# Optimization experiments

Hardware: AMD Instinct MI355X
Metric: run time of the kernel (lower is better)

Reference implementation:

```python
import jax, jax.numpy as jnp
import numpy as np

B, S, D, H = 2, 2048, 1024, 16
DK = D // H


def setup_inputs() -> dict:
    key = jax.random.key(0)
    ks = jax.random.split(key, 8)
    scale = 1.0 / np.sqrt(D)
    inp = {
        "query": jax.random.normal(ks[0], (B, S, D), dtype=jnp.float32),
        "key": jax.random.normal(ks[1], (B, S, D), dtype=jnp.float32),
        "value": jax.random.normal(ks[2], (B, S, D), dtype=jnp.float32),
        # causal mask, broadcastable over batch and heads
        "mask": jnp.tril(jnp.ones((S, S), dtype=jnp.int32))[None, None, :, :],
        "W_q": jax.random.normal(ks[3], (D, D), dtype=jnp.float32) * scale,
        "W_k": jax.random.normal(ks[4], (D, D), dtype=jnp.float32) * scale,
        "W_v": jax.random.normal(ks[5], (D, D), dtype=jnp.float32) * scale,
        "W_o": jax.random.normal(ks[6], (D, D), dtype=jnp.float32) * scale,
    }
    return inp


def _split_heads(t):
    Bb, Ss, _ = t.shape
    return t.reshape(Bb, Ss, H, DK).transpose(0, 2, 1, 3)  # [B,H,S,DK]


def reference(query, key, value, mask, W_q, W_k, W_v, W_o):
    # Linear(d,d,bias=False): y = x @ W^T (torch stores weight as [out,in])
    Q = _split_heads(query @ W_q.T)
    K = _split_heads(key @ W_k.T)
    V = _split_heads(value @ W_v.T)
    scores = jnp.einsum("bhqd,bhkd->bhqk", Q, K) / jnp.sqrt(jnp.float32(DK))
    scores = jnp.where(mask == 0, -jnp.inf, scores)
    weights = jax.nn.softmax(scores, axis=-1)
    weights = jnp.nan_to_num(weights, nan=0.0)  # fully-masked rows -> 0
    # dropout is identity at inference
    x = jnp.einsum("bhqk,bhkd->bhqd", weights, V)
    x = x.transpose(0, 2, 1, 3).reshape(B, S, D)
    return x @ W_o.T
```

## Files before the change

### kernel.cpp

```cpp
#include <hip/hip_runtime.h>
#include <hip/hip_bf16.h>

#define D_MODEL 1024
#define NHEAD   16
#define HDK     64
#define SEQ     2048
#define BATCH   2
#define BS      (BATCH * SEQ)

typedef __attribute__((ext_vector_type(8))) short bf16x8;
typedef __attribute__((ext_vector_type(4))) float f32x4;

__device__ __forceinline__ unsigned short f2bf(float f) {
    unsigned u = __builtin_bit_cast(unsigned, f);
    u += 0x7fffu + ((u >> 16) & 1u);
    return (unsigned short)(u >> 16);
}

__device__ __forceinline__ unsigned pack_hi(float x, float y) {
    return __builtin_amdgcn_perm(__builtin_bit_cast(unsigned, y),
                                 __builtin_bit_cast(unsigned, x), 0x07060302u);
}

typedef const void __attribute__((address_space(1))) gas_void;
typedef void __attribute__((address_space(3))) las_void;

__device__ __forceinline__ void gll16(const void* g, void* l) {
    __builtin_amdgcn_global_load_lds((gas_void*)g, (las_void*)l, 16, 0, 0);
}

__device__ __forceinline__ void cast_body(const float* __restrict__ src,
                                          unsigned short* __restrict__ dst, int i) {
    const float4* p = (const float4*)src + (size_t)i * 2;
    float4 a = p[0], b = p[1];
    ushort4 lo = make_ushort4(f2bf(a.x), f2bf(a.y), f2bf(a.z), f2bf(a.w));
    ushort4 hi = make_ushort4(f2bf(b.x), f2bf(b.y), f2bf(b.z), f2bf(b.w));
    ushort4* q = (ushort4*)dst + (size_t)i * 2;
    q[0] = lo; q[1] = hi;
}

__global__ __launch_bounds__(256)
void cast_act(const float* a, const float* b, const float* c,
              unsigned short* oa, unsigned short* ob, unsigned short* oc, int n8) {
    int i = blockIdx.x * 256 + threadIdx.x;
    if (i >= n8) return;
    const float* s = blockIdx.y == 0 ? a : blockIdx.y == 1 ? b : c;
    unsigned short* d = blockIdx.y == 0 ? oa : blockIdx.y == 1 ? ob : oc;
    cast_body(s, d, i);
}

__global__ __launch_bounds__(256)
void cast_wt(const float* a, const float* b, const float* c, const float* dd,
             unsigned short* oa, unsigned short* ob, unsigned short* oc, unsigned short* od, int n8) {
    int i = blockIdx.x * 256 + threadIdx.x;
    if (i >= n8) return;
    const float* s = blockIdx.y == 0 ? a : blockIdx.y == 1 ? b : blockIdx.y == 2 ? c : dd;
    unsigned short* d = blockIdx.y == 0 ? oa : blockIdx.y == 1 ? ob : blockIdx.y == 2 ? oc : od;
    cast_body(s, d, i);
}

__device__ __forceinline__ void gemm_kloop128(const unsigned short* __restrict__ X,
                                              const unsigned short* __restrict__ W,
                                              unsigned short* As, unsigned short* Bs,
                                              int bm, int bn, f32x4 acc[4][4]) {
    const int t    = threadIdx.x;
    const int w    = t >> 6;
    const int L    = t & 63;
    const int quad = L >> 4;
    const int lm   = L & 15;
    const int r8   = L >> 3;
    const int sl   = L & 7;
    const int xcol = ((sl ^ r8) & 7) * 8;
    const int wr   = (w >> 1) * 64;
    const int wc   = (w & 1) * 64;

    for (int kt = 0; kt < D_MODEL; kt += 64) {
        __syncthreads();
        #pragma unroll
        for (int i = 0; i < 4; ++i) {
            int c = w * 4 + i;
            gll16(X + (size_t)(bm + c * 8 + r8) * D_MODEL + kt + xcol, &As[c * 512]);
        }
        #pragma unroll
        for (int i = 0; i < 4; ++i) {
            int c = w * 4 + i;
            gll16(W + (size_t)(bn + c * 8 + r8) * D_MODEL + kt + xcol, &Bs[c * 512]);
        }
        __syncthreads();

        #pragma unroll
        for (int ch = 0; ch < 2; ++ch) {
            bf16x8 af[4], bfr[4];
            #pragma unroll
            for (int ms = 0; ms < 4; ++ms) {
                int row = wr + ms * 16 + lm;
                af[ms] = *(const bf16x8*)&As[row * 64 + (((ch * 4 + quad) ^ (row & 7)) * 8)];
            }
            #pragma unroll
            for (int ns = 0; ns < 4; ++ns) {
                int row = wc + ns * 16 + lm;
                bfr[ns] = *(const bf16x8*)&Bs[row * 64 + (((ch * 4 + quad) ^ (row & 7)) * 8)];
            }
            #pragma unroll
            for (int ms = 0; ms < 4; ++ms)
                #pragma unroll
                for (int ns = 0; ns < 4; ++ns)
                    acc[ms][ns] = __builtin_amdgcn_mfma_f32_16x16x32_bf16(
                        af[ms], bfr[ns], acc[ms][ns], 0, 0, 0);
        }
    }
}

__device__ __forceinline__ void gemm_kloop64(const unsigned short* __restrict__ X,
                                             const unsigned short* __restrict__ W,
                                             unsigned short* As, unsigned short* Bs,
                                             int bm, int bn, f32x4 acc[2][4]) {
    const int t    = threadIdx.x;
    const int w    = t >> 6;
    const int L    = t & 63;
    const int quad = L >> 4;
    const int lm   = L & 15;
    const int r8   = L >> 3;
    const int sl   = L & 7;
    const int xcol = ((sl ^ r8) & 7) * 8;

    for (int kt = 0; kt < D_MODEL; kt += 64) {
        __syncthreads();
        #pragma unroll
        for (int i = 0; i < 4; ++i) {
            int c = w * 4 + i;
            gll16(X + (size_t)(bm + c * 8 + r8) * D_MODEL + kt + xcol, &As[c * 512]);
        }
        #pragma unroll
        for (int i = 0; i < 2; ++i) {
            int c = w * 2 + i;
            gll16(W + (size_t)(bn + c * 8 + r8) * D_MODEL + kt + xcol, &Bs[c * 512]);
        }
        __syncthreads();

        #pragma unroll
        for (int ch = 0; ch < 2; ++ch) {
            bf16x8 af[2], bfr[4];
            #pragma unroll
            for (int ms = 0; ms < 2; ++ms) {
                int row = w * 32 + ms * 16 + lm;
                af[ms] = *(const bf16x8*)&As[row * 64 + (((ch * 4 + quad) ^ (row & 7)) * 8)];
            }
            #pragma unroll
            for (int ns = 0; ns < 4; ++ns) {
                int row = ns * 16 + lm;
                bfr[ns] = *(const bf16x8*)&Bs[row * 64 + (((ch * 4 + quad) ^ (row & 7)) * 8)];
            }
            #pragma unroll
            for (int ms = 0; ms < 2; ++ms)
                #pragma unroll
                for (int ns = 0; ns < 4; ++ns)
                    acc[ms][ns] = __builtin_amdgcn_mfma_f32_16x16x32_bf16(
                        af[ms], bfr[ns], acc[ms][ns], 0, 0, 0);
        }
    }
}

__global__ __launch_bounds__(256, 3)
void proj_gemm(const unsigned short* __restrict__ qx, const unsigned short* __restrict__ kx,
               const unsigned short* __restrict__ vx, const unsigned short* __restrict__ wq,
               const unsigned short* __restrict__ wk, const unsigned short* __restrict__ wv,
               unsigned short* __restrict__ Qp, unsigned short* __restrict__ Kp,
               unsigned short* __restrict__ VT) {
    __shared__ __align__(16) unsigned short As[128 * 64];
    __shared__ __align__(16) unsigned short Bs[128 * 64];

    const int p = blockIdx.z;
    const unsigned short* X = p == 0 ? qx : p == 1 ? kx : vx;
    const unsigned short* W = p == 0 ? wq : p == 1 ? wk : wv;
    const int bm = blockIdx.y * 128, bn = blockIdx.x * 128;

    f32x4 acc[4][4];
    #pragma unroll
    for (int ms = 0; ms < 4; ++ms)
        #pragma unroll
        for (int ns = 0; ns < 4; ++ns)
            acc[ms][ns] = (f32x4){0.f, 0.f, 0.f, 0.f};

    gemm_kloop128(X, W, As, Bs, bm, bn, acc);

    const int t = threadIdx.x, w = t >> 6, L = t & 63, quad = L >> 4, lm = L & 15;
    const int wr = (w >> 1) * 64, wc = (w & 1) * 64;
    if (p == 2) {
        const int b    = bm >> 11;
        const int s_in = (bm & (SEQ - 1)) + wr;
        #pragma unroll
        for (int ms = 0; ms < 4; ++ms)
            #pragma unroll
            for (int ns = 0; ns < 4; ++ns) {
                int dg = bn + wc + ns * 16 + lm;
                int h  = dg >> 6, d = dg & 63;
                ushort4 pk = make_ushort4(f2bf(acc[ms][ns][0]), f2bf(acc[ms][ns][1]),
                                          f2bf(acc[ms][ns][2]), f2bf(acc[ms][ns][3]));
                *(ushort4*)&VT[((size_t)((b * NHEAD + h) * HDK + d)) * SEQ +
                               s_in + ms * 16 + quad * 4] = pk;
            }
    } else {
        unsigned short* Y = p == 0 ? Qp : Kp;
        const float scl = p == 0 ? 0.125f : 1.0f;
        #pragma unroll
        for (int ms = 0; ms < 4; ++ms)
            #pragma unroll
            for (int ns = 0; ns < 4; ++ns)
                #pragma unroll
                for (int r = 0; r < 4; ++r)
                    Y[(size_t)(bm + wr + ms * 16 + quad * 4 + r) * D_MODEL +
                      bn + wc + ns * 16 + lm] = f2bf(acc[ms][ns][r] * scl);
    }
}

__global__ __launch_bounds__(256)
void out_gemm(const unsigned short* __restrict__ X, const unsigned short* __restrict__ W,
              float* __restrict__ Y) {
    __shared__ __align__(16) unsigned short As[128 * 64];
    __shared__ __align__(16) unsigned short Bs[64 * 64];
    const int bm = blockIdx.y * 128, bn = blockIdx.x * 64;

    f32x4 acc[2][4];
    #pragma unroll
    for (int ms = 0; ms < 2; ++ms)
        #pragma unroll
        for (int ns = 0; ns < 4; ++ns)
            acc[ms][ns] = (f32x4){0.f, 0.f, 0.f, 0.f};

    gemm_kloop64(X, W, As, Bs, bm, bn, acc);

    const int t = threadIdx.x, w = t >> 6, L = t & 63, quad = L >> 4, lm = L & 15;
    #pragma unroll
    for (int ms = 0; ms < 2; ++ms)
        #pragma unroll
        for (int ns = 0; ns < 4; ++ns)
            #pragma unroll
            for (int r = 0; r < 4; ++r)
                Y[(size_t)(bm + w * 32 + ms * 16 + quad * 4 + r) * D_MODEL +
                  bn + ns * 16 + lm] = acc[ms][ns][r];
}

__global__ __launch_bounds__(128)
void attn_mfma(const unsigned short* __restrict__ Q, const unsigned short* __restrict__ K,
               const unsigned short* __restrict__ VT, unsigned short* __restrict__ A) {
    __shared__ __align__(16) unsigned short Ks[2][64 * 64];
    __shared__ __align__(16) unsigned short Vs[2][64 * 64];
    __shared__ __align__(16) unsigned short Qs[64 * 64];
    __shared__ __align__(16) unsigned short Ps[2][16 * 68];

    const int t    = threadIdx.x;
    const int w    = t >> 6;
    const int L    = t & 63;
    const int quad = L >> 4;
    const int lm   = L & 15;
    const int r8   = L >> 3;
    const int xcol = ((L & 7) ^ r8) * 8;

    const int f    = blockIdx.x;
    const int g    = (f & 7) + ((f >> 7) << 3);
    const int pidx = (f >> 3) & 15;
    const int b    = g >> 4, h = g & 15;
    const size_t hb  = (size_t)b * SEQ * D_MODEL + h * HDK;
    const size_t vhb = (size_t)(b * NHEAD + h) * HDK;

    unsigned short* ps = &Ps[w][0];

    for (int half = 0; half < 2; ++half) {
        const int qt = half ? 31 - pidx : pidx;
        const int q0 = qt * 64;

        #pragma unroll
        for (int i = 0; i < 4; ++i) {
            int c = w * 4 + i;
            gll16(Q + hb + (size_t)(q0 + c * 8 + r8) * D_MODEL + xcol, &Qs[c * 512]);
            gll16(K + hb + (size_t)(c * 8 + r8) * D_MODEL + xcol, &Ks[0][c * 512]);
            gll16(VT + (vhb + c * 8 + r8) * SEQ + xcol, &Vs[0][c * 512]);
        }
        __syncthreads();

        bf16x8 Qf[2][2];
        #pragma unroll
        for (int s = 0; s < 2; ++s) {
            int row = w * 32 + s * 16 + lm;
            Qf[s][0] = *(const bf16x8*)&Qs[row * 64 + ((quad ^ (row & 7)) * 8)];
            Qf[s][1] = *(const bf16x8*)&Qs[row * 64 + (((4 + quad) ^ (row & 7)) * 8)];
        }

        f32x4 Oacc[2][4];
        #pragma unroll
        for (int s = 0; s < 2; ++s)
            #pragma unroll
            for (int nt = 0; nt < 4; ++nt)
                Oacc[s][nt] = (f32x4){0.f, 0.f, 0.f, 0.f};
        float m_run[2] = {-INFINITY, -INFINITY};
        float l_run[2] = {0.f, 0.f};

        int bb = 0;
        for (int kt = 0; kt <= qt; ++kt) {
            if (kt < qt) {
                #pragma unroll
                for (int i = 0; i < 4; ++i) {
                    int c = w * 4 + i;
                    gll16(K + hb + (size_t)((kt + 1) * 64 + c * 8 + r8) * D_MODEL + xcol,
                          &Ks[bb ^ 1][c * 512]);
                    gll16(VT + (vhb + c * 8 + r8) * SEQ + (kt + 1) * 64 + xcol,
                          &Vs[bb ^ 1][c * 512]);
                }
            }
            const unsigned short* Kc = Ks[bb];
            const unsigned short* Vc = Vs[bb];

            bf16x8 Kf[4][2], Vf[4][2];
            #pragma unroll
            for (int ct = 0; ct < 4; ++ct) {
                int row = ct * 16 + lm;
                int o0  = row * 64 + ((quad ^ (row & 7)) * 8);
                int o1  = row * 64 + (((4 + quad) ^ (row & 7)) * 8);
                Kf[ct][0] = *(const bf16x8*)&Kc[o0];
                Kf[ct][1] = *(const bf16x8*)&Kc[o1];
                Vf[ct][0] = *(const bf16x8*)&Vc[o0];
                Vf[ct][1] = *(const bf16x8*)&Vc[o1];
            }

            #pragma unroll
            for (int s = 0; s < 2; ++s) {
                const int qrow = q0 + w * 32 + s * 16 + lm;
                f32x4 S[4];
                #pragma unroll
                for (int ct = 0; ct < 4; ++ct) {
                    f32x4 z = (f32x4){0.f, 0.f, 0.f, 0.f};
                    z = __builtin_amdgcn_mfma_f32_16x16x32_bf16(Kf[ct][0], Qf[s][0], z, 0, 0, 0);
                    z = __builtin_amdgcn_mfma_f32_16x16x32_bf16(Kf[ct][1], Qf[s][1], z, 0, 0, 0);
                    S[ct] = z;
                }

                if (kt == qt) {
                    #pragma unroll
                    for (int ct = 0; ct < 4; ++ct)
                        #pragma unroll
                        for (int r = 0; r < 4; ++r)
                            if ((q0 + ct * 16 + quad * 4 + r) > qrow)
                                S[ct][r] = -1e30f;
                }

                float m = fmaxf(fmaxf(fmaxf(S[0][0], S[0][1]), fmaxf(S[0][2], S[0][3])),
                                fmaxf(fmaxf(S[1][0], S[1][1]), fmaxf(S[1][2], S[1][3])));
                m = fmaxf(m, fmaxf(fmaxf(fmaxf(S[2][0], S[2][1]), fmaxf(S[2][2], S[2][3])),
                                   fmaxf(fmaxf(S[3][0], S[3][1]), fmaxf(S[3][2], S[3][3]))));
                m = fmaxf(m, __shfl_xor(m, 16));
                m = fmaxf(m, __shfl_xor(m, 32));
                const float m_new = fmaxf(m_run[s], m);
                const float alpha = __expf(m_run[s] - m_new);
                m_run[s] = m_new;
                float psum = 0.f;
                #pragma unroll
                for (int ct = 0; ct < 4; ++ct)
                    #pragma unroll
                    for (int r = 0; r < 4; ++r) {
                        float e = __expf(S[ct][r] - m_new);
                        S[ct][r] = e;
                        psum += e;
                    }
                psum += __shfl_xor(psum, 16);
                psum += __shfl_xor(psum, 32);
                l_run[s] = l_run[s] * alpha + psum;

                #pragma unroll
                for (int ct = 0; ct < 4; ++ct) {
                    uint2 pw = make_uint2(pack_hi(S[ct][0], S[ct][1]),
                                          pack_hi(S[ct][2], S[ct][3]));
                    *(uint2*)&ps[lm * 68 + ct * 16 + quad * 4] = pw;
                }
                bf16x8 Pb0 = *(const bf16x8*)&ps[lm * 68 + quad * 8];
                bf16x8 Pb1 = *(const bf16x8*)&ps[lm * 68 + 32 + quad * 8];

                #pragma unroll
                for (int nt = 0; nt < 4; ++nt) {
                    f32x4 o = Oacc[s][nt];
                    #pragma unroll
                    for (int r = 0; r < 4; ++r) o[r] *= alpha;
                    o = __builtin_amdgcn_mfma_f32_16x16x32_bf16(Vf[nt][0], Pb0, o, 0, 0, 0);
                    o = __builtin_amdgcn_mfma_f32_16x16x32_bf16(Vf[nt][1], Pb1, o, 0, 0, 0);
                    Oacc[s][nt] = o;
                }
            }

            __syncthreads();
            bb ^= 1;
        }

        #pragma unroll
        for (int s = 0; s < 2; ++s) {
            const float inv_l = 1.f / l_run[s];
            #pragma unroll
            for (int nt = 0; nt < 4; ++nt) {
                ushort4 pk = make_ushort4(f2bf(Oacc[s][nt][0] * inv_l),
                                          f2bf(Oacc[s][nt][1] * inv_l),
                                          f2bf(Oacc[s][nt][2] * inv_l),
                                          f2bf(Oacc[s][nt][3] * inv_l));
                *(ushort4*)&ps[lm * 68 + nt * 16 + quad * 4] = pk;
            }
            #pragma unroll
            for (int cc = 0; cc < 2; ++cc) {
                int chunk = cc * 64 + L;
                int row = chunk >> 3, seg = chunk & 7;
                uint4 val = *(const uint4*)&ps[row * 68 + seg * 8];
                *(uint4*)&A[hb + (size_t)(q0 + w * 32 + s * 16 + row) * D_MODEL + seg * 8] = val;
            }
        }
    }
}

extern "C" void kernel_launch(void* const* d_in, const int* in_sizes, int n_in,
                              void* d_out, int out_size, void* d_ws, size_t ws_size,
                              hipStream_t stream) {
    const float* q  = (const float*)d_in[0];
    const float* k  = (const float*)d_in[1];
    const float* v  = (const float*)d_in[2];
    const float* Wq = (const float*)d_in[4];
    const float* Wk = (const float*)d_in[5];
    const float* Wv = (const float*)d_in[6];
    const float* Wo = (const float*)d_in[7];
    float* out = (float*)d_out;

    char* ws = (char*)d_ws;
    const size_t MB = 1024 * 1024;
    unsigned short* qb  = (unsigned short*)(ws + 0 * MB);
    unsigned short* kb  = (unsigned short*)(ws + 8 * MB);
    unsigned short* vb  = (unsigned short*)(ws + 16 * MB);
    unsigned short* wqb = (unsigned short*)(ws + 24 * MB);
    unsigned short* wkb = (unsigned short*)(ws + 26 * MB);
    unsigned short* wvb = (unsigned short*)(ws + 28 * MB);
    unsigned short* wob = (unsigned short*)(ws + 30 * MB);
    unsigned short* Qp  = (unsigned short*)(ws + 32 * MB);
    unsigned short* Kp  = (unsigned short*)(ws + 40 * MB);
    unsigned short* VTp = (unsigned short*)(ws + 48 * MB);
    unsigned short* Ap  = (unsigned short*)(ws + 56 * MB);

    const int nX8 = BS * D_MODEL / 8;
    const int nW8 = D_MODEL * D_MODEL / 8;
    cast_act<<<dim3(nX8 / 256, 3), 256, 0, stream>>>(q, k, v, qb, kb, vb, nX8);
    cast_wt <<<dim3(nW8 / 256, 4), 256, 0, stream>>>(Wq, Wk, Wv, Wo, wqb, wkb, wvb, wob, nW8);

    proj_gemm<<<dim3(D_MODEL / 128, BS / 128, 3), 256, 0, stream>>>(
        qb, kb, vb, wqb, wkb, wvb, Qp, Kp, VTp);

    attn_mfma<<<dim3(512), 128, 0, stream>>>(Qp, Kp, VTp, Ap);

    out_gemm<<<dim3(D_MODEL / 64, BS / 128), 256, 0, stream>>>(Ap, wob, out);
}
```

Measured before the change: 242.8 us.

## Split attention into one block per query tile, fold log2e scale, merge casts

The attention kernel now launches one block per (query tile, batch-head) pair, ordered longest-first, instead of pairing two tiles per block. This gives 1024 blocks and should balance the causal workload across CUs. Q fragments are loaded straight from global memory into registers, which drops the Q shared-memory tile. The log2(e) factor is folded into the Q projection scale so the softmax can use the hardware exp2. The two cast kernels are merged into a single launch. In exchange, each K/V tile is reloaded by twice as many blocks, and each block pays its own setup cost.

```diff
diff --git a/kernel.cpp b/kernel.cpp
--- a/kernel.cpp
+++ b/kernel.cpp
@@ -22,6 +22,14 @@
                                  __builtin_bit_cast(unsigned, x), 0x07060302u);
 }
 
+__device__ __forceinline__ float fexp2(float x) {
+#if __has_builtin(__builtin_amdgcn_exp2f)
+    return __builtin_amdgcn_exp2f(x);
+#else
+    return exp2f(x);
+#endif
+}
+
 typedef const void __attribute__((address_space(1))) gas_void;
 typedef void __attribute__((address_space(3))) las_void;
 
@@ -29,34 +37,32 @@
     __builtin_amdgcn_global_load_lds((gas_void*)g, (las_void*)l, 16, 0, 0);
 }
 
-__device__ __forceinline__ void cast_body(const float* __restrict__ src,
-                                          unsigned short* __restrict__ dst, int i) {
-    const float4* p = (const float4*)src + (size_t)i * 2;
+__global__ __launch_bounds__(256)
+void cast_all(const float* q, const float* k, const float* v,
+              const float* wq, const float* wk, const float* wv, const float* wo,
+              unsigned short* oq, unsigned short* ok, unsigned short* ov,
+              unsigned short* owq, unsigned short* owk, unsigned short* owv,
+              unsigned short* owo, int nact8, int nwt8) {
+    const int y = blockIdx.y;
+    const int n8 = y < 3 ? nact8 : nwt8;
+    int i = blockIdx.x * 256 + threadIdx.x;
+    if (i >= n8) return;
+    const float* s; unsigned short* d;
+    switch (y) {
+        case 0: s = q;  d = oq;  break;
+        case 1: s = k;  d = ok;  break;
+        case 2: s = v;  d = ov;  break;
+        case 3: s = wq; d = owq; break;
+        case 4: s = wk; d = owk; break;
+        case 5: s = wv; d = owv; break;
+        default: s = wo; d = owo; break;
+    }
+    const float4* p = (const float4*)s + (size_t)i * 2;
     float4 a = p[0], b = p[1];
     ushort4 lo = make_ushort4(f2bf(a.x), f2bf(a.y), f2bf(a.z), f2bf(a.w));
     ushort4 hi = make_ushort4(f2bf(b.x), f2bf(b.y), f2bf(b.z), f2bf(b.w));
-    ushort4* q = (ushort4*)dst + (size_t)i * 2;
-    q[0] = lo; q[1] = hi;
-}
-
-__global__ __launch_bounds__(256)
-void cast_act(const float* a, const float* b, const float* c,
-              unsigned short* oa, unsigned short* ob, unsigned short* oc, int n8) {
-    int i = blockIdx.x * 256 + threadIdx.x;
-    if (i >= n8) return;
-    const float* s = blockIdx.y == 0 ? a : blockIdx.y == 1 ? b : c;
-    unsigned short* d = blockIdx.y == 0 ? oa : blockIdx.y == 1 ? ob : oc;
-    cast_body(s, d, i);
-}
-
-__global__ __launch_bounds__(256)
-void cast_wt(const float* a, const float* b, const float* c, const float* dd,
-             unsigned short* oa, unsigned short* ob, unsigned short* oc, unsigned short* od, int n8) {
-    int i = blockIdx.x * 256 + threadIdx.x;
-    if (i >= n8) return;
-    const float* s = blockIdx.y == 0 ? a : blockIdx.y == 1 ? b : blockIdx.y == 2 ? c : dd;
-    unsigned short* d = blockIdx.y == 0 ? oa : blockIdx.y == 1 ? ob : blockIdx.y == 2 ? oc : od;
-    cast_body(s, d, i);
+    ushort4* o = (ushort4*)d + (size_t)i * 2;
+    o[0] = lo; o[1] = hi;
 }
 
 __device__ __forceinline__ void gemm_kloop128(const unsigned short* __restrict__ X,
@@ -202,7 +208,7 @@
             }
     } else {
         unsigned short* Y = p == 0 ? Qp : Kp;
-        const float scl = p == 0 ? 0.125f : 1.0f;
+        const float scl = p == 0 ? 0.18033688011112042f : 1.0f;
         #pragma unroll
         for (int ms = 0; ms < 4; ++ms)
             #pragma unroll
@@ -246,7 +252,6 @@
                const unsigned short* __restrict__ VT, unsigned short* __restrict__ A) {
     __shared__ __align__(16) unsigned short Ks[2][64 * 64];
     __shared__ __align__(16) unsigned short Vs[2][64 * 64];
-    __shared__ __align__(16) unsigned short Qs[64 * 64];
     __shared__ __align__(16) unsigned short Ps[2][16 * 68];
 
     const int t    = threadIdx.x;
@@ -258,156 +263,152 @@
     const int xcol = ((L & 7) ^ r8) * 8;
 
     const int f    = blockIdx.x;
-    const int g    = (f & 7) + ((f >> 7) << 3);
-    const int pidx = (f >> 3) & 15;
-    const int b    = g >> 4, h = g & 15;
+    const int qt   = 31 - (f >> 5);
+    const int bh   = f & 31;
+    const int b    = bh >> 4, h = bh & 15;
+    const int q0   = qt * 64;
     const size_t hb  = (size_t)b * SEQ * D_MODEL + h * HDK;
     const size_t vhb = (size_t)(b * NHEAD + h) * HDK;
 
     unsigned short* ps = &Ps[w][0];
 
-    for (int half = 0; half < 2; ++half) {
-        const int qt = half ? 31 - pidx : pidx;
-        const int q0 = qt * 64;
-
-        #pragma unroll
-        for (int i = 0; i < 4; ++i) {
-            int c = w * 4 + i;
-            gll16(Q + hb + (size_t)(q0 + c * 8 + r8) * D_MODEL + xcol, &Qs[c * 512]);
-            gll16(K + hb + (size_t)(c * 8 + r8) * D_MODEL + xcol, &Ks[0][c * 512]);
-            gll16(VT + (vhb + c * 8 + r8) * SEQ + xcol, &Vs[0][c * 512]);
-        }
-        __syncthreads();
-
-        bf16x8 Qf[2][2];
+    bf16x8 Qf[2][2];
+    #pragma unroll
+    for (int s = 0; s < 2; ++s) {
+        const unsigned short* qp =
+            Q + hb + (size_t)(q0 + w * 32 + s * 16 + lm) * D_MODEL + quad * 8;
+        Qf[s][0] = *(const bf16x8*)qp;
+        Qf[s][1] = *(const bf16x8*)(qp + 32);
+    }
+
+    f32x4 Oacc[2][4];
+    #pragma unroll
+    for (int s = 0; s < 2; ++s)
+        #pragma unroll
+        for (int nt = 0; nt < 4; ++nt)
+            Oacc[s][nt] = (f32x4){0.f, 0.f, 0.f, 0.f};
+    float m_run[2] = {-INFINITY, -INFINITY};
+    float l_run[2] = {0.f, 0.f};
+
+    #pragma unroll
+    for (int i = 0; i < 4; ++i) {
+        int c = w * 4 + i;
+        gll16(K + hb + (size_t)(c * 8 + r8) * D_MODEL + xcol, &Ks[0][c * 512]);
+        gll16(VT + (vhb + c * 8 + r8) * SEQ + xcol, &Vs[0][c * 512]);
+    }
+    __syncthreads();
+
+    int bb = 0;
+    for (int kt = 0; kt <= qt; ++kt) {
+        if (kt < qt) {
+            #pragma unroll
+            for (int i = 0; i < 4; ++i) {
+                int c = w * 4 + i;
+                gll16(K + hb + (size_t)((kt + 1) * 64 + c * 8 + r8) * D_MODEL + xcol,
+                      &Ks[bb ^ 1][c * 512]);
+                gll16(VT + (vhb + c * 8 + r8) * SEQ + (kt + 1) * 64 + xcol,
+                      &Vs[bb ^ 1][c * 512]);
+            }
+        }
+        const unsigned short* Kc = Ks[bb];
+        const unsigned short* Vc = Vs[bb];
+
+        bf16x8 Kf[4][2], Vf[4][2];
+        #pragma unroll
+        for (int ct = 0; ct < 4; ++ct) {
+            int row = ct * 16 + lm;
+            int o0  = row * 64 + ((quad ^ (row & 7)) * 8);
+            int o1  = row * 64 + (((4 + quad) ^ (row & 7)) * 8);
+            Kf[ct][0] = *(const bf16x8*)&Kc[o0];
+            Kf[ct][1] = *(const bf16x8*)&Kc[o1];
+            Vf[ct][0] = *(const bf16x8*)&Vc[o0];
+            Vf[ct][1] = *(const bf16x8*)&Vc[o1];
+        }
+
         #pragma unroll
         for (int s = 0; s < 2; ++s) {
-            int row = w * 32 + s * 16 + lm;
-            Qf[s][0] = *(const bf16x8*)&Qs[row * 64 + ((quad ^ (row & 7)) * 8)];
-            Qf[s][1] = *(const bf16x8*)&Qs[row * 64 + (((4 + quad) ^ (row & 7)) * 8)];
-        }
-
-        f32x4 Oacc[2][4];
-        #pragma unroll
-        for (int s = 0; s < 2; ++s)
-            #pragma unroll
-            for (int nt = 0; nt < 4; ++nt)
-                Oacc[s][nt] = (f32x4){0.f, 0.f, 0.f, 0.f};
-        float m_run[2] = {-INFINITY, -INFINITY};
-        float l_run[2] = {0.f, 0.f};
-
-        int bb = 0;
-        for (int kt = 0; kt <= qt; ++kt) {
-            if (kt < qt) {
-                #pragma unroll
-                for (int i = 0; i < 4; ++i) {
-                    int c = w * 4 + i;
-                    gll16(K + hb + (size_t)((kt + 1) * 64 + c * 8 + r8) * D_MODEL + xcol,
-                          &Ks[bb ^ 1][c * 512]);
-                    gll16(VT + (vhb + c * 8 + r8) * SEQ + (kt + 1) * 64 + xcol,
-                          &Vs[bb ^ 1][c * 512]);
-                }
-            }
-            const unsigned short* Kc = Ks[bb];
-            const unsigned short* Vc = Vs[bb];
-
-            bf16x8 Kf[4][2], Vf[4][2];
+            const int qrow = q0 + w * 32 + s * 16 + lm;
+            f32x4 S[4];
             #pragma unroll
             for (int ct = 0; ct < 4; ++ct) {
-                int row = ct * 16 + lm;
-                int o0  = row * 64 + ((quad ^ (row & 7)) * 8);
-                int o1  = row * 64 + (((4 + quad) ^ (row & 7)) * 8);
-                Kf[ct][0] = *(const bf16x8*)&Kc[o0];
-                Kf[ct][1] = *(const bf16x8*)&Kc[o1];
-                Vf[ct][0] = *(const bf16x8*)&Vc[o0];
-                Vf[ct][1] = *(const bf16x8*)&Vc[o1];
-            }
-
-            #pragma unroll
-            for (int s = 0; s < 2; ++s) {
-                const int qrow = q0 + w * 32 + s * 16 + lm;
-                f32x4 S[4];
-                #pragma unroll
-                for (int ct = 0; ct < 4; ++ct) {
-                    f32x4 z = (f32x4){0.f, 0.f, 0.f, 0.f};
-                    z = __builtin_amdgcn_mfma_f32_16x16x32_bf16(Kf[ct][0], Qf[s][0], z, 0, 0, 0);
-                    z = __builtin_amdgcn_mfma_f32_16x16x32_bf16(Kf[ct][1], Qf[s][1], z, 0, 0, 0);
-                    S[ct] = z;
-                }
-
-                if (kt == qt) {
-                    #pragma unroll
-                    for (int ct = 0; ct < 4; ++ct)
-                        #pragma unroll
-                        for (int r = 0; r < 4; ++r)
-                            if ((q0 + ct * 16 + quad * 4 + r) > qrow)
-                                S[ct][r] = -1e30f;
-                }
-
-                float m = fmaxf(fmaxf(fmaxf(S[0][0], S[0][1]), fmaxf(S[0][2], S[0][3])),
-                                fmaxf(fmaxf(S[1][0], S[1][1]), fmaxf(S[1][2], S[1][3])));
-                m = fmaxf(m, fmaxf(fmaxf(fmaxf(S[2][0], S[2][1]), fmaxf(S[2][2], S[2][3])),
-                                   fmaxf(fmaxf(S[3][0], S[3][1]), fmaxf(S[3][2], S[3][3]))));
-                m = fmaxf(m, __shfl_xor(m, 16));
-                m = fmaxf(m, __shfl_xor(m, 32));
-                const float m_new = fmaxf(m_run[s], m);
-                const float alpha = __expf(m_run[s] - m_new);
-                m_run[s] = m_new;
-                float psum = 0.f;
+                f32x4 z = (f32x4){0.f, 0.f, 0.f, 0.f};
+                z = __builtin_amdgcn_mfma_f32_16x16x32_bf16(Kf[ct][0], Qf[s][0], z, 0, 0, 0);
+                z = __builtin_amdgcn_mfma_f32_16x16x32_bf16(Kf[ct][1], Qf[s][1], z, 0, 0, 0);
+                S[ct] = z;
+            }
+
+            if (kt == qt) {
                 #pragma unroll
                 for (int ct = 0; ct < 4; ++ct)
                     #pragma unroll
-                    for (int r = 0; r < 4; ++r) {
-                        float e = __expf(S[ct][r] - m_new);
-                        S[ct][r] = e;
-                        psum += e;
-                    }
-                psum += __shfl_xor(psum, 16);
-                psum += __shfl_xor(psum, 32);
-                l_run[s] = l_run[s] * alpha + psum;
-
-                #pragma unroll
-                for (int ct = 0; ct < 4; ++ct) {
-                    uint2 pw = make_uint2(pack_hi(S[ct][0], S[ct][1]),
-                                          pack_hi(S[ct][2], S[ct][3]));
-                    *(uint2*)&ps[lm * 68 + ct * 16 + quad * 4] = pw;
+                    for (int r = 0; r < 4; ++r)
+                        if ((q0 + ct * 16 + quad * 4 + r) > qrow)
+                            S[ct][r] = -1e30f;
+            }
+
+            float m = fmaxf(fmaxf(fmaxf(S[0][0], S[0][1]), fmaxf(S[0][2], S[0][3])),
+                            fmaxf(fmaxf(S[1][0], S[1][1]), fmaxf(S[1][2], S[1][3])));
+            m = fmaxf(m, fmaxf(fmaxf(fmaxf(S[2][0], S[2][1]), fmaxf(S[2][2], S[2][3])),
+                               fmaxf(fmaxf(S[3][0], S[3][1]), fmaxf(S[3][2], S[3][3]))));
+            m = fmaxf(m, __shfl_xor(m, 16));
+            m = fmaxf(m, __shfl_xor(m, 32));
+            const float m_new = fmaxf(m_run[s], m);
+            const float alpha = fexp2(m_run[s] - m_new);
+            m_run[s] = m_new;
+            float psum = 0.f;
+            #pragma unroll
+            for (int ct = 0; ct < 4; ++ct)
+                #pragma unroll
+                for (int r = 0; r < 4; ++r) {
+                    float e = fexp2(S[ct][r] - m_new);
+                    S[ct][r] = e;
+                    psum += e;
                 }
-                bf16x8 Pb0 = *(const bf16x8*)&ps[lm * 68 + quad * 8];
-                bf16x8 Pb1 = *(const bf16x8*)&ps[lm * 68 + 32 + quad * 8];
-
-                #pragma unroll
-                for (int nt = 0; nt < 4; ++nt) {
-                    f32x4 o = Oacc[s][nt];
-                    #pragma unroll
-                    for (int r = 0; r < 4; ++r) o[r] *= alpha;
-                    o = __builtin_amdgcn_mfma_f32_16x16x32_bf16(Vf[nt][0], Pb0, o, 0, 0, 0);
-                    o = __builtin_amdgcn_mfma_f32_16x16x32_bf16(Vf[nt][1], Pb1, o, 0, 0, 0);
-                    Oacc[s][nt] = o;
-                }
-            }
-
-            __syncthreads();
-            bb ^= 1;
-        }
-
-        #pragma unroll
-        for (int s = 0; s < 2; ++s) {
-            const float inv_l = 1.f / l_run[s];
+            psum += __shfl_xor(psum, 16);
+            psum += __shfl_xor(psum, 32);
+            l_run[s] = l_run[s] * alpha + psum;
+
+            #pragma unroll
+            for (int ct = 0; ct < 4; ++ct) {
+                uint2 pw = make_uint2(pack_hi(S[ct][0], S[ct][1]),
+                                      pack_hi(S[ct][2], S[ct][3]));
+                *(uint2*)&ps[lm * 68 + ct * 16 + quad * 4] = pw;
+            }
+            bf16x8 Pb0 = *(const bf16x8*)&ps[lm * 68 + quad * 8];
+            bf16x8 Pb1 = *(const bf16x8*)&ps[lm * 68 + 32 + quad * 8];
+
             #pragma unroll
             for (int nt = 0; nt < 4; ++nt) {
-                ushort4 pk = make_ushort4(f2bf(Oacc[s][nt][0] * inv_l),
-                                          f2bf(Oacc[s][nt][1] * inv_l),
-                                          f2bf(Oacc[s][nt][2] * inv_l),
-                                          f2bf(Oacc[s][nt][3] * inv_l));
-                *(ushort4*)&ps[lm * 68 + nt * 16 + quad * 4] = pk;
-            }
-            #pragma unroll
-            for (int cc = 0; cc < 2; ++cc) {
-                int chunk = cc * 64 + L;
-                int row = chunk >> 3, seg = chunk & 7;
-                uint4 val = *(const uint4*)&ps[row * 68 + seg * 8];
-                *(uint4*)&A[hb + (size_t)(q0 + w * 32 + s * 16 + row) * D_MODEL + seg * 8] = val;
-            }
+                f32x4 o = Oacc[s][nt];
+                #pragma unroll
+                for (int r = 0; r < 4; ++r) o[r] *= alpha;
+                o = __builtin_amdgcn_mfma_f32_16x16x32_bf16(Vf[nt][0], Pb0, o, 0, 0, 0);
+                o = __builtin_amdgcn_mfma_f32_16x16x32_bf16(Vf[nt][1], Pb1, o, 0, 0, 0);
+                Oacc[s][nt] = o;
+            }
+        }
+
+        __syncthreads();
+        bb ^= 1;
+    }
+
+    #pragma unroll
+    for (int s = 0; s < 2; ++s) {
+        const float inv_l = 1.f / l_run[s];
+        #pragma unroll
+        for (int nt = 0; nt < 4; ++nt) {
+            ushort4 pk = make_ushort4(f2bf(Oacc[s][nt][0] * inv_l),
+                                      f2bf(Oacc[s][nt][1] * inv_l),
+                                      f2bf(Oacc[s][nt][2] * inv_l),
+                                      f2bf(Oacc[s][nt][3] * inv_l));
+            *(ushort4*)&ps[lm * 68 + nt * 16 + quad * 4] = pk;
+        }
+        #pragma unroll
+        for (int cc = 0; cc < 2; ++cc) {
+            int chunk = cc * 64 + L;
+            int row = chunk >> 3, seg = chunk & 7;
+            uint4 val = *(const uint4*)&ps[row * 68 + seg * 8];
+            *(uint4*)&A[hb + (size_t)(q0 + w * 32 + s * 16 + row) * D_MODEL + seg * 8] = val;
         }
     }
 }
@@ -440,13 +441,13 @@
 
     const int nX8 = BS * D_MODEL / 8;
     const int nW8 = D_MODEL * D_MODEL / 8;
-    cast_act<<<dim3(nX8 / 256, 3), 256, 0, stream>>>(q, k, v, qb, kb, vb, nX8);
-    cast_wt <<<dim3(nW8 / 256, 4), 256, 0, stream>>>(Wq, Wk, Wv, Wo, wqb, wkb, wvb, wob, nW8);
+    cast_all<<<dim3(nX8 / 256, 7), 256, 0, stream>>>(
+        q, k, v, Wq, Wk, Wv, Wo, qb, kb, vb, wqb, wkb, wvb, wob, nX8, nW8);
 
     proj_gemm<<<dim3(D_MODEL / 128, BS / 128, 3), 256, 0, stream>>>(
         qb, kb, vb, wqb, wkb, wvb, Qp, Kp, VTp);
 
-    attn_mfma<<<dim3(512), 128, 0, stream>>>(Qp, Kp, VTp, Ap);
+    attn_mfma<<<dim3(1024), 128, 0, stream>>>(Qp, Kp, VTp, Ap);
 
     out_gemm<<<dim3(D_MODEL / 64, BS / 128), 256, 0, stream>>>(Ap, wob, out);
 }
```

Measured after the change: 236.3 us. -2.7%, faster.
